# Optimization experiments

Hardware: AMD Instinct MI355X
Metric: run time of the kernel (lower is better)

## Reference

```python
import jax, jax.numpy as jnp
import numpy as np

B, C, F, H, W = 8, 16, 256, 112, 112   # batch, cells/image, channels, height, width
NB = 3                                  # tgt_shape = (3, 3) adaptive pool bins


def setup_inputs() -> dict:
    key = jax.random.key(0)
    kf, ky, kx, kry, krx, kn = jax.random.split(key, 6)
    feature_maps = jax.random.normal(kf, (B, F, H, W), jnp.float32)
    N = B * C
    # random rectangular cell blobs with bernoulli interior holes + guaranteed core
    cy = jax.random.randint(ky, (N, 1, 1), 20, H - 20)
    cx = jax.random.randint(kx, (N, 1, 1), 20, W - 20)
    ry = jax.random.randint(kry, (N, 1, 1), 5, 18)
    rx = jax.random.randint(krx, (N, 1, 1), 5, 18)
    yy = jnp.arange(H)[None, :, None]
    xx = jnp.arange(W)[None, None, :]
    rect = (jnp.abs(yy - cy) <= ry) & (jnp.abs(xx - cx) <= rx)
    noise = jax.random.bernoulli(kn, 0.8, (N, H, W))
    core = (jnp.abs(yy - cy) <= 2) & (jnp.abs(xx - cx) <= 2)
    cell_masks = rect & (noise | core)            # [N, H, W] bool, each nonempty
    cell_counts = jnp.full((B,), C, jnp.int32)    # fixed cells per image
    return {"feature_maps": feature_maps, "cell_masks": cell_masks,
            "cell_counts": cell_counts}


def _bin_membership(lo, hi, length):
    # adaptive-pool bin i covers [lo + floor(i*sz/NB), lo + ceil((i+1)*sz/NB))
    i = jnp.arange(NB)
    sz = (hi - lo)[..., None]                      # [B, C, 1]
    start = lo[..., None] + (i * sz) // NB         # [B, C, NB]
    end = lo[..., None] + ((i + 1) * sz + NB - 1) // NB
    pos = jnp.arange(length)
    return (pos >= start[..., None]) & (pos < end[..., None])  # [B, C, NB, L]


def reference(feature_maps, cell_masks, cell_counts):
    Bv, Fv, Hv, Wv = feature_maps.shape
    Cv = cell_masks.shape[0] // Bv
    masks = cell_masks.reshape(Bv, Cv, Hv, Wv)
    # tight bbox per cell (first/last True row and column, exclusive end)
    rows = masks.any(-1)                            # [B, C, H]
    cols = masks.any(-2)                            # [B, C, W]
    y0 = jnp.argmax(rows, -1)
    y1 = Hv - jnp.argmax(rows[..., ::-1], -1)
    x0 = jnp.argmax(cols, -1)
    x1 = Wv - jnp.argmax(cols[..., ::-1], -1)
    ymem = _bin_membership(y0, y1, Hv)              # [B, C, NB, H]
    xmem = _bin_membership(x0, x1, Wv)              # [B, C, NB, W]
    neg = jnp.finfo(feature_maps.dtype).min
    feat = feature_maps[:, None]                    # [B, 1, F, H, W]
    m = masks[:, :, None]                           # [B, C, 1, H, W]
    pooled = []
    for i in range(NB):
        ym = ymem[:, :, i][:, :, None, :, None]     # [B, C, 1, H, 1]
        for j in range(NB):
            xm = xmem[:, :, j][:, :, None, None, :]  # [B, C, 1, 1, W]
            inbin = ym & xm
            # inside bin & mask -> feature; inside bin & ~mask -> 0 (zeroed crop);
            # outside bin -> -inf (excluded from max)
            v = jnp.where(inbin & m, feat, jnp.where(inbin, 0.0, neg))
            pooled.append(v.max((-1, -2)))          # [B, C, F]
    out = jnp.stack(pooled, -1)                     # [B, C, F, 9], index = i*NB + j
    # matches torch pooled.view(-1): flatten order f*9 + i*3 + j
    return out.reshape(Bv * Cv, Fv * NB * NB)
```

## Files before the change

### kernel.cpp

```cpp
#include <hip/hip_runtime.h>
#include <float.h>

#define B_  8
#define C_  16
#define N_  (B_*C_)
#define F_  256
#define H_  112
#define W_  112
#define HW_ (H_*W_)
#define NB_ 3

#define RB_STRIDE 40
#define NPACK 14


__global__ __launch_bounds__(256) void bbox_kernel(const int4* __restrict__ mask4,
                                                   int* __restrict__ bb,
                                                   unsigned long long* __restrict__ rowbits) {
    int n = blockIdx.x, t = threadIdx.x;
    const int4* m = mask4 + (size_t)n * (HW_ / 4);
    int ymin = 1 << 20, ymax = -1, xmin = 1 << 20, xmax = -1;
    for (int i = t; i < HW_ / 4; i += 256) {
        int4 v = m[i];
        int y = i / 28;
        int xb = (i - y * 28) * 4;
        if (v.x | v.y | v.z | v.w) { ymin = min(ymin, y); ymax = max(ymax, y); }
        if (v.x) { xmin = min(xmin, xb);     xmax = max(xmax, xb);     }
        if (v.y) { xmin = min(xmin, xb + 1); xmax = max(xmax, xb + 1); }
        if (v.z) { xmin = min(xmin, xb + 2); xmax = max(xmax, xb + 2); }
        if (v.w) { xmin = min(xmin, xb + 3); xmax = max(xmax, xb + 3); }
    }
    #pragma unroll
    for (int off = 32; off; off >>= 1) {
        ymin = min(ymin, __shfl_xor(ymin, off));
        ymax = max(ymax, __shfl_xor(ymax, off));
        xmin = min(xmin, __shfl_xor(xmin, off));
        xmax = max(xmax, __shfl_xor(xmax, off));
    }
    __shared__ int red[4][4];
    __shared__ int sb[3];
    int wave = t >> 6;
    if ((t & 63) == 0) {
        red[wave][0] = ymin; red[wave][1] = ymax;
        red[wave][2] = xmin; red[wave][3] = xmax;
    }
    __syncthreads();
    if (t == 0) {
        for (int w = 1; w < 4; ++w) {
            ymin = min(ymin, red[w][0]); ymax = max(ymax, red[w][1]);
            xmin = min(xmin, red[w][2]); xmax = max(xmax, red[w][3]);
        }
        int y0 = ymin, y1 = ymax + 1, x0 = xmin, x1 = xmax + 1;
        int* o = bb + n * 16;
        o[0] = y0; o[1] = y1; o[2] = x0; o[3] = x1;
        int szy = y1 - y0, szx = x1 - x0;
        for (int i = 0; i < NB_; ++i) {
            o[4+i]  = y0 + (i*szy)/NB_;
            o[7+i]  = y0 + ((i+1)*szy + NB_-1)/NB_;
            o[10+i] = x0 + (i*szx)/NB_;
            o[13+i] = x0 + ((i+1)*szx + NB_-1)/NB_;
        }
        sb[0] = y0; sb[1] = szy; sb[2] = x0 & ~3;
    }
    __syncthreads();
    {
        int y0 = sb[0], bh = sb[1], x0a = sb[2];
        int lane = t & 63;
        const int* mrow = (const int*)mask4 + (size_t)n * HW_ + x0a + lane;
        for (int dy = wave; dy < bh; dy += 4) {
            int v = mrow[(size_t)(y0 + dy) * W_];
            unsigned long long bits = __ballot(v != 0);
            if (lane == 0) rowbits[n * RB_STRIDE + dy] = bits;
        }
    }
}

__global__ __launch_bounds__(256, 4) void pool_kernel(
        const float* __restrict__ feat,
        const unsigned long long* __restrict__ rowbits,
        const int* __restrict__ bb, float* __restrict__ out) {
    int n = blockIdx.x;
    int b = n >> 4;
    const int* o = bb + n * 16;
    int y0 = o[0], x0 = o[2];
    int bw = o[3] - x0;
    int x0a = x0 & ~3;
    int wbw = (x0 - x0a) + bw;

    int lane = threadIdx.x & 63, wave = threadIdx.x >> 6;
    int xq = lane & 15, rg = lane >> 4;
    int bi = min(rg, 2);
    int xq4 = (4 * xq < wbw) ? 4 * xq : 0;
    int f = blockIdx.y * 4 + wave;
    const float* gp = feat + (size_t)(b * F_ + f) * HW_ + (size_t)y0 * W_ + x0a + xq4;

    int ysb  = o[4 + bi];
    int yeb1 = o[7 + bi] - 1;

    unsigned long long mynib = 0;
    {
        const unsigned long long* rbp = rowbits + n * RB_STRIDE;
        #pragma unroll
        for (int u = 0; u < NPACK; ++u) {
            int dy = min(ysb + u, yeb1) - y0;
            unsigned long long row = rbp[dy];
            mynib |= ((row >> (4 * xq)) & 0xFull) << (4 * u);
        }
    }

    float4 cr[NPACK];
    #pragma unroll
    for (int u = 0; u < NPACK; ++u) {
        int off = (min(ysb + u, yeb1) - y0) * W_;
        cr[u] = *(const float4*)(gp + off);
    }

    float acc[4];
    #pragma unroll
    for (int s = 0; s < 4; ++s) acc[s] = -FLT_MAX;

    #pragma unroll
    for (int u = 0; u < NPACK; ++u) {
        unsigned int nib = (unsigned int)(mynib >> (4 * u)) & 0xFu;
        acc[0] = fmaxf(acc[0], (nib & 1u) ? cr[u].x : 0.f);
        acc[1] = fmaxf(acc[1], (nib & 2u) ? cr[u].y : 0.f);
        acc[2] = fmaxf(acc[2], (nib & 4u) ? cr[u].z : 0.f);
        acc[3] = fmaxf(acc[3], (nib & 8u) ? cr[u].w : 0.f);
    }

    int xg = x0a + 4 * xq;
    float part[3];
    #pragma unroll
    for (int j = 0; j < 3; ++j) {
        int xs = o[10 + j], xe = o[13 + j];
        float r = -FLT_MAX;
        #pragma unroll
        for (int s = 0; s < 4; ++s) {
            int xx = xg + s;
            float lim = (xx >= xs && xx < xe) ? FLT_MAX : -FLT_MAX;
            r = fmaxf(r, fminf(acc[s], lim));
        }
        part[j] = r;
    }
    #pragma unroll
    for (int off = 1; off <= 8; off <<= 1) {
        #pragma unroll
        for (int j = 0; j < 3; ++j)
            part[j] = fmaxf(part[j], __shfl_xor(part[j], off));
    }
    if (xq == 0 && rg < 3) {
        float* op = out + (size_t)(n * F_ + f) * 9 + rg * 3;
        op[0] = part[0]; op[1] = part[1]; op[2] = part[2];
    }
}

extern "C" void kernel_launch(void* const* d_in, const int* in_sizes, int n_in,
                              void* d_out, int out_size, void* d_ws, size_t ws_size,
                              hipStream_t stream) {
    const float* feat = (const float*)d_in[0];
    const int*   mask = (const int*)d_in[1];
    int* bb = (int*)d_ws;
    unsigned long long* rowbits = (unsigned long long*)((char*)d_ws + 8192);

    bbox_kernel<<<N_, 256, 0, stream>>>((const int4*)mask, bb, rowbits);
    dim3 grid(N_, F_ / 4);
    pool_kernel<<<grid, 256, 0, stream>>>(feat, rowbits, bb, (float*)d_out);
}
```

Before: 183.0 us.

## Stage full feature planes in LDS and share across all cells of an image

Each block now handles one image and eight feature channels, loading whole 112x112 planes into double-buffered shared memory with coalesced float4 loads. All 16 cells of the image then pool from the LDS copy instead of each cell gathering its own bbox rows from global memory. The next plane's global loads are issued before computing on the current one to overlap transfer and compute. This trades redundant scattered global reads for large LDS usage and fewer, bigger blocks, which lowers occupancy.

Result: slower. 211.2 us (+15.4%).

```diff
diff --git a/kernel.cpp b/kernel.cpp
--- a/kernel.cpp
+++ b/kernel.cpp
@@ -12,6 +12,10 @@
 
 #define RB_STRIDE 40
 #define NPACK 14
+
+#define LPITCH 116
+#define FPB    8
+#define NCHUNK 49
 
 
 __global__ __launch_bounds__(256) void bbox_kernel(const int4* __restrict__ mask4,
@@ -75,83 +79,120 @@
     }
 }
 
-__global__ __launch_bounds__(256, 4) void pool_kernel(
+__global__ __launch_bounds__(512, 2) void pool_kernel(
         const float* __restrict__ feat,
         const unsigned long long* __restrict__ rowbits,
         const int* __restrict__ bb, float* __restrict__ out) {
-    int n = blockIdx.x;
-    int b = n >> 4;
-    const int* o = bb + n * 16;
-    int y0 = o[0], x0 = o[2];
-    int bw = o[3] - x0;
-    int x0a = x0 & ~3;
-    int wbw = (x0 - x0a) + bw;
-
-    int lane = threadIdx.x & 63, wave = threadIdx.x >> 6;
+    __shared__ float buf[2][112 * LPITCH];
+
+    int bid = blockIdx.x;
+    int b  = bid >> 5;
+    int f0 = (bid & 31) * FPB;
+
+    int tid = threadIdx.x;
+    int lane = tid & 63, w = tid >> 6;
     int xq = lane & 15, rg = lane >> 4;
     int bi = min(rg, 2);
-    int xq4 = (4 * xq < wbw) ? 4 * xq : 0;
-    int f = blockIdx.y * 4 + wave;
-    const float* gp = feat + (size_t)(b * F_ + f) * HW_ + (size_t)y0 * W_ + x0a + xq4;
-
-    int ysb  = o[4 + bi];
-    int yeb1 = o[7 + bi] - 1;
-
-    unsigned long long mynib = 0;
-    {
+
+    int ysb[2], yeb1[2], lcol[2], xgc[2];
+    int xs[2][3], xe[2][3];
+    unsigned long long mynib[2];
+    #pragma unroll
+    for (int cc = 0; cc < 2; ++cc) {
+        int n = b * C_ + 2 * w + cc;
+        const int* o = bb + n * 16;
+        int y0 = o[0], x0 = o[2];
+        int bw = o[3] - x0;
+        int x0a = x0 & ~3;
+        int wbw = (x0 - x0a) + bw;
+        int xq4 = (4 * xq < wbw) ? 4 * xq : 0;
+        ysb[cc]  = o[4 + bi];
+        yeb1[cc] = o[7 + bi] - 1;
+        lcol[cc] = x0a + xq4;
+        xgc[cc]  = x0a + 4 * xq;
+        #pragma unroll
+        for (int j = 0; j < 3; ++j) { xs[cc][j] = o[10 + j]; xe[cc][j] = o[13 + j]; }
+        unsigned long long nib = 0;
         const unsigned long long* rbp = rowbits + n * RB_STRIDE;
         #pragma unroll
         for (int u = 0; u < NPACK; ++u) {
-            int dy = min(ysb + u, yeb1) - y0;
-            unsigned long long row = rbp[dy];
-            mynib |= ((row >> (4 * xq)) & 0xFull) << (4 * u);
-        }
-    }
-
-    float4 cr[NPACK];
-    #pragma unroll
-    for (int u = 0; u < NPACK; ++u) {
-        int off = (min(ysb + u, yeb1) - y0) * W_;
-        cr[u] = *(const float4*)(gp + off);
-    }
-
-    float acc[4];
-    #pragma unroll
-    for (int s = 0; s < 4; ++s) acc[s] = -FLT_MAX;
-
-    #pragma unroll
-    for (int u = 0; u < NPACK; ++u) {
-        unsigned int nib = (unsigned int)(mynib >> (4 * u)) & 0xFu;
-        acc[0] = fmaxf(acc[0], (nib & 1u) ? cr[u].x : 0.f);
-        acc[1] = fmaxf(acc[1], (nib & 2u) ? cr[u].y : 0.f);
-        acc[2] = fmaxf(acc[2], (nib & 4u) ? cr[u].z : 0.f);
-        acc[3] = fmaxf(acc[3], (nib & 8u) ? cr[u].w : 0.f);
-    }
-
-    int xg = x0a + 4 * xq;
-    float part[3];
-    #pragma unroll
-    for (int j = 0; j < 3; ++j) {
-        int xs = o[10 + j], xe = o[13 + j];
-        float r = -FLT_MAX;
+            int dy = min(ysb[cc] + u, yeb1[cc]) - y0;
+            nib |= ((rbp[dy] >> (4 * xq)) & 0xFull) << (4 * u);
+        }
+        mynib[cc] = nib;
+    }
+
+    const float* fbase = feat + (size_t)(b * F_ + f0) * HW_;
+    float4 v[7];
+    #define ISSUE(p)                                                        \
+        { const float* fp = fbase + (size_t)(p) * HW_;                      \
+          _Pragma("unroll")                                                 \
+          for (int k = 0; k < 7; ++k) {                                     \
+              int ch = k * 8 + w;                                           \
+              if (ch < NCHUNK) v[k] = *(const float4*)(fp + 4*(ch*64+lane)); } }
+    #define WRLDS(pb)                                                       \
+        { float* dst = buf[pb];                                             \
+          _Pragma("unroll")                                                 \
+          for (int k = 0; k < 7; ++k) {                                     \
+              int ch = k * 8 + w;                                           \
+              if (ch < NCHUNK) {                                            \
+                  int i = ch * 64 + lane;                                   \
+                  int r = i / 28, c4 = i - 28 * r;                          \
+                  *(float4*)(dst + r * LPITCH + 4 * c4) = v[k]; } } }
+
+    ISSUE(0);
+    WRLDS(0);
+    __syncthreads();
+
+    for (int p = 0; p < FPB; ++p) {
+        if (p + 1 < FPB) ISSUE(p + 1);
+
+        const float* bp = buf[p & 1];
         #pragma unroll
-        for (int s = 0; s < 4; ++s) {
-            int xx = xg + s;
-            float lim = (xx >= xs && xx < xe) ? FLT_MAX : -FLT_MAX;
-            r = fmaxf(r, fminf(acc[s], lim));
-        }
-        part[j] = r;
-    }
-    #pragma unroll
-    for (int off = 1; off <= 8; off <<= 1) {
-        #pragma unroll
-        for (int j = 0; j < 3; ++j)
-            part[j] = fmaxf(part[j], __shfl_xor(part[j], off));
-    }
-    if (xq == 0 && rg < 3) {
-        float* op = out + (size_t)(n * F_ + f) * 9 + rg * 3;
-        op[0] = part[0]; op[1] = part[1]; op[2] = part[2];
-    }
+        for (int cc = 0; cc < 2; ++cc) {
+            float4 cr[NPACK];
+            #pragma unroll
+            for (int u = 0; u < NPACK; ++u) {
+                int row = min(ysb[cc] + u, yeb1[cc]);
+                cr[u] = *(const float4*)(bp + row * LPITCH + lcol[cc]);
+            }
+            float a0 = -FLT_MAX, a1 = -FLT_MAX, a2 = -FLT_MAX, a3 = -FLT_MAX;
+            #pragma unroll
+            for (int u = 0; u < NPACK; ++u) {
+                unsigned int nib = (unsigned int)(mynib[cc] >> (4 * u)) & 0xFu;
+                a0 = fmaxf(a0, (nib & 1u) ? cr[u].x : 0.f);
+                a1 = fmaxf(a1, (nib & 2u) ? cr[u].y : 0.f);
+                a2 = fmaxf(a2, (nib & 4u) ? cr[u].z : 0.f);
+                a3 = fmaxf(a3, (nib & 8u) ? cr[u].w : 0.f);
+            }
+            float part[3];
+            #pragma unroll
+            for (int j = 0; j < 3; ++j) {
+                int xx = xgc[cc];
+                float r;
+                r = fminf(a0, (xx     >= xs[cc][j] && xx     < xe[cc][j]) ? FLT_MAX : -FLT_MAX);
+                r = fmaxf(r, fminf(a1, (xx + 1 >= xs[cc][j] && xx + 1 < xe[cc][j]) ? FLT_MAX : -FLT_MAX));
+                r = fmaxf(r, fminf(a2, (xx + 2 >= xs[cc][j] && xx + 2 < xe[cc][j]) ? FLT_MAX : -FLT_MAX));
+                r = fmaxf(r, fminf(a3, (xx + 3 >= xs[cc][j] && xx + 3 < xe[cc][j]) ? FLT_MAX : -FLT_MAX));
+                part[j] = r;
+            }
+            #pragma unroll
+            for (int off = 1; off <= 8; off <<= 1)
+                #pragma unroll
+                for (int j = 0; j < 3; ++j)
+                    part[j] = fmaxf(part[j], __shfl_xor(part[j], off));
+            if (xq == 0 && rg < 3) {
+                int n = b * C_ + 2 * w + cc;
+                float* op = out + (size_t)(n * F_ + f0 + p) * 9 + rg * 3;
+                op[0] = part[0]; op[1] = part[1]; op[2] = part[2];
+            }
+        }
+
+        if (p + 1 < FPB) WRLDS((p + 1) & 1);
+        __syncthreads();
+    }
+    #undef ISSUE
+    #undef WRLDS
 }
 
 extern "C" void kernel_launch(void* const* d_in, const int* in_sizes, int n_in,
@@ -163,6 +204,5 @@
     unsigned long long* rowbits = (unsigned long long*)((char*)d_ws + 8192);
 
     bbox_kernel<<<N_, 256, 0, stream>>>((const int4*)mask, bb, rowbits);
-    dim3 grid(N_, F_ / 4);
-    pool_kernel<<<grid, 256, 0, stream>>>(feat, rowbits, bb, (float*)d_out);
+    pool_kernel<<<N_ * 2, 512, 0, stream>>>(feat, rowbits, bb, (float*)d_out);
 }
```

## Process an 8-channel strip per wave, reusing per-cell setup across channels

Applied to the files above, without the earlier changes.

Each wave now handles eight consecutive feature channels of one cell instead of a single channel, and the grid is flattened to 1024 blocks. The per-cell setup (bbox reads, row-bit nibble packing, row offsets, x-bin limit masks) is computed once and reused across the eight channels. This amortizes setup and the dependent bb/rowbits loads. In exchange there are eight times fewer waves, so less memory-level parallelism from concurrent waves, and the channel loop is not unrolled.

Result: faster. 169.1 us (-7.6%).

```diff
diff --git a/kernel.cpp b/kernel.cpp
--- a/kernel.cpp
+++ b/kernel.cpp
@@ -12,6 +12,7 @@
 
 #define RB_STRIDE 40
 #define NPACK 14
+#define FSTRIP 8
 
 
 __global__ __launch_bounds__(256) void bbox_kernel(const int4* __restrict__ mask4,
@@ -79,23 +80,31 @@
         const float* __restrict__ feat,
         const unsigned long long* __restrict__ rowbits,
         const int* __restrict__ bb, float* __restrict__ out) {
-    int n = blockIdx.x;
-    int b = n >> 4;
+    int tid  = threadIdx.x;
+    int lane = tid & 63, w = tid >> 6;
+    int gw = blockIdx.x * 4 + w;
+    int n  = gw >> 5;
+    int f0 = (gw & 31) * FSTRIP;
+    int b  = n >> 4;
+
     const int* o = bb + n * 16;
     int y0 = o[0], x0 = o[2];
     int bw = o[3] - x0;
     int x0a = x0 & ~3;
     int wbw = (x0 - x0a) + bw;
 
-    int lane = threadIdx.x & 63, wave = threadIdx.x >> 6;
     int xq = lane & 15, rg = lane >> 4;
     int bi = min(rg, 2);
     int xq4 = (4 * xq < wbw) ? 4 * xq : 0;
-    int f = blockIdx.y * 4 + wave;
-    const float* gp = feat + (size_t)(b * F_ + f) * HW_ + (size_t)y0 * W_ + x0a + xq4;
+    const float* gp = feat + (size_t)(b * F_ + f0) * HW_ + (size_t)y0 * W_ + x0a + xq4;
 
     int ysb  = o[4 + bi];
     int yeb1 = o[7 + bi] - 1;
+
+    int roff[NPACK];
+    #pragma unroll
+    for (int u = 0; u < NPACK; ++u)
+        roff[u] = (min(ysb + u, yeb1) - y0) * W_;
 
     unsigned long long mynib = 0;
     {
@@ -103,54 +112,59 @@
         #pragma unroll
         for (int u = 0; u < NPACK; ++u) {
             int dy = min(ysb + u, yeb1) - y0;
-            unsigned long long row = rbp[dy];
-            mynib |= ((row >> (4 * xq)) & 0xFull) << (4 * u);
+            mynib |= ((rbp[dy] >> (4 * xq)) & 0xFull) << (4 * u);
         }
     }
 
-    float4 cr[NPACK];
-    #pragma unroll
-    for (int u = 0; u < NPACK; ++u) {
-        int off = (min(ysb + u, yeb1) - y0) * W_;
-        cr[u] = *(const float4*)(gp + off);
-    }
-
-    float acc[4];
-    #pragma unroll
-    for (int s = 0; s < 4; ++s) acc[s] = -FLT_MAX;
-
-    #pragma unroll
-    for (int u = 0; u < NPACK; ++u) {
-        unsigned int nib = (unsigned int)(mynib >> (4 * u)) & 0xFu;
-        acc[0] = fmaxf(acc[0], (nib & 1u) ? cr[u].x : 0.f);
-        acc[1] = fmaxf(acc[1], (nib & 2u) ? cr[u].y : 0.f);
-        acc[2] = fmaxf(acc[2], (nib & 4u) ? cr[u].z : 0.f);
-        acc[3] = fmaxf(acc[3], (nib & 8u) ? cr[u].w : 0.f);
-    }
-
     int xg = x0a + 4 * xq;
-    float part[3];
+    float lim[3][4];
     #pragma unroll
     for (int j = 0; j < 3; ++j) {
         int xs = o[10 + j], xe = o[13 + j];
-        float r = -FLT_MAX;
         #pragma unroll
         for (int s = 0; s < 4; ++s) {
             int xx = xg + s;
-            float lim = (xx >= xs && xx < xe) ? FLT_MAX : -FLT_MAX;
-            r = fmaxf(r, fminf(acc[s], lim));
+            lim[j][s] = (xx >= xs && xx < xe) ? FLT_MAX : -FLT_MAX;
         }
-        part[j] = r;
     }
-    #pragma unroll
-    for (int off = 1; off <= 8; off <<= 1) {
+
+    for (int ff = 0; ff < FSTRIP; ++ff) {
+        float4 cr[NPACK];
         #pragma unroll
-        for (int j = 0; j < 3; ++j)
-            part[j] = fmaxf(part[j], __shfl_xor(part[j], off));
-    }
-    if (xq == 0 && rg < 3) {
-        float* op = out + (size_t)(n * F_ + f) * 9 + rg * 3;
-        op[0] = part[0]; op[1] = part[1]; op[2] = part[2];
+        for (int u = 0; u < NPACK; ++u)
+            cr[u] = *(const float4*)(gp + roff[u]);
+
+        float a0 = -FLT_MAX, a1 = -FLT_MAX, a2 = -FLT_MAX, a3 = -FLT_MAX;
+        #pragma unroll
+        for (int u = 0; u < NPACK; ++u) {
+            unsigned int nib = (unsigned int)(mynib >> (4 * u)) & 0xFu;
+            a0 = fmaxf(a0, (nib & 1u) ? cr[u].x : 0.f);
+            a1 = fmaxf(a1, (nib & 2u) ? cr[u].y : 0.f);
+            a2 = fmaxf(a2, (nib & 4u) ? cr[u].z : 0.f);
+            a3 = fmaxf(a3, (nib & 8u) ? cr[u].w : 0.f);
+        }
+
+        float part[3];
+        #pragma unroll
+        for (int j = 0; j < 3; ++j) {
+            float r;
+            r = fminf(a0, lim[j][0]);
+            r = fmaxf(r, fminf(a1, lim[j][1]));
+            r = fmaxf(r, fminf(a2, lim[j][2]));
+            r = fmaxf(r, fminf(a3, lim[j][3]));
+            part[j] = r;
+        }
+        #pragma unroll
+        for (int off = 1; off <= 8; off <<= 1) {
+            #pragma unroll
+            for (int j = 0; j < 3; ++j)
+                part[j] = fmaxf(part[j], __shfl_xor(part[j], off));
+        }
+        if (xq == 0 && rg < 3) {
+            float* op = out + (size_t)(n * F_ + f0 + ff) * 9 + rg * 3;
+            op[0] = part[0]; op[1] = part[1]; op[2] = part[2];
+        }
+        gp += HW_;
     }
 }
 
@@ -163,6 +177,5 @@
     unsigned long long* rowbits = (unsigned long long*)((char*)d_ws + 8192);
 
     bbox_kernel<<<N_, 256, 0, stream>>>((const int4*)mask, bb, rowbits);
-    dim3 grid(N_, F_ / 4);
-    pool_kernel<<<grid, 256, 0, stream>>>(feat, rowbits, bb, (float*)d_out);
+    pool_kernel<<<1024, 256, 0, stream>>>(feat, rowbits, bb, (float*)d_out);
 }
```
